# Performance work log

Hardware: AMD Instinct MI355X
Metric: run time of the kernel (lower is better)

Reference implementation:

```python
import jax, jax.numpy as jnp
import numpy as np

D_MODEL = 1024
N_HEADS = 16
D_K = D_MODEL // N_HEADS
CAUSAL = True


def setup_inputs() -> dict:
    key = jax.random.key(0)
    ks = jax.random.split(key, 11)
    B, S, D = 2, 2048, D_MODEL
    scale = 1.0 / np.sqrt(D)
    inp = {
        "in_Q": jax.random.normal(ks[0], (B, S, D), jnp.float32),
        "in_K": jax.random.normal(ks[1], (B, S, D), jnp.float32),
        "in_V": jax.random.normal(ks[2], (B, S, D), jnp.float32),
        # torch Linear params: weight [out, in], bias [out]
        "Wq": jax.random.normal(ks[3], (D, D), jnp.float32) * scale,
        "bq": jax.random.normal(ks[4], (D,), jnp.float32) * scale,
        "Wk": jax.random.normal(ks[5], (D, D), jnp.float32) * scale,
        "bk": jax.random.normal(ks[6], (D,), jnp.float32) * scale,
        "Wv": jax.random.normal(ks[7], (D, D), jnp.float32) * scale,
        "bv": jax.random.normal(ks[8], (D,), jnp.float32) * scale,
        "Wo": jax.random.normal(ks[9], (D, D), jnp.float32) * scale,
        "bo": jax.random.normal(ks[10], (D,), jnp.float32) * scale,
    }
    return inp


def reference(in_Q, in_K, in_V, Wq, bq, Wk, bk, Wv, bv, Wo, bo):
    B, S, D = in_Q.shape
    H, dk = N_HEADS, D_K
    # Linear projections (torch: x @ W.T + b)
    Q = in_Q @ Wq.T + bq
    K = in_K @ Wk.T + bk
    V = in_V @ Wv.T + bv
    # split heads: [B, S, D] -> [B, H, S, dk]
    Qh = Q.reshape(B, S, H, dk).transpose(0, 2, 1, 3)
    Kh = K.reshape(B, S, H, dk).transpose(0, 2, 1, 3)
    Vh = V.reshape(B, S, H, dk).transpose(0, 2, 1, 3)
    # scores [B, H, S, S]
    scores = jnp.einsum("bhqd,bhkd->bhqk", Qh, Kh) / jnp.sqrt(jnp.float32(dk))
    if CAUSAL:
        mask = jnp.tril(jnp.ones((S, S), dtype=bool))
        scores = jnp.where(mask, scores, -jnp.inf)
    attn = jax.nn.softmax(scores, axis=-1)
    out = jnp.einsum("bhqk,bhkd->bhqd", attn, Vh)
    Hcat = out.transpose(0, 2, 1, 3).reshape(B, S, D)
    return Hcat @ Wo.T + bo
```

## Files before the change

kernel.cpp:

```cpp
#include <hip/hip_runtime.h>
#include <hip/hip_bf16.h>
#include <math.h>

#define D_MODEL 1024
#define NHEADS  16
#define DK      64
#define SEQ     2048
#define BATCH   2
#define MROWS   4096
#define NQT     (SEQ/64)

typedef unsigned short ushort_t;
using short8 = __attribute__((ext_vector_type(8))) short;
using f32x4  = __attribute__((ext_vector_type(4))) float;

__device__ __forceinline__ ushort_t f2bf(float x) {
    unsigned u = __float_as_uint(x);
    u = (u + 0x7FFFu + ((u >> 16) & 1u)) >> 16;
    return (ushort_t)u;
}

__device__ __forceinline__ unsigned pk2(float a, float b) {
    __hip_bfloat162 h = __float22bfloat162_rn(float2{a, b});
    unsigned u;
    __builtin_memcpy(&u, &h, 4);
    return u;
}

__device__ __forceinline__ void gll16(const ushort_t* g, ushort_t* l) {
    __builtin_amdgcn_global_load_lds(
        (const __attribute__((address_space(1))) void*)(g),
        (__attribute__((address_space(3))) void*)(l), 16, 0, 0);
}

__global__ __launch_bounds__(256) void cvt_bf16(
    const float* s0, const float* s1, const float* s2, const float* s3,
    const float* s4, const float* s5, const float* s6,
    ushort_t* d0, ushort_t* d1, ushort_t* d2, ushort_t* d3,
    ushort_t* d4, ushort_t* d5, ushort_t* d6, int nIn, int nW)
{
    const float* s; ushort_t* d; int n;
    switch (blockIdx.y) {
        case 0: s = s0; d = d0; n = nIn; break;
        case 1: s = s1; d = d1; n = nIn; break;
        case 2: s = s2; d = d2; n = nIn; break;
        case 3: s = s3; d = d3; n = nW;  break;
        case 4: s = s4; d = d4; n = nW;  break;
        case 5: s = s5; d = d5; n = nW;  break;
        default: s = s6; d = d6; n = nW; break;
    }
    int i = (blockIdx.x * 256 + threadIdx.x) * 4;
    if (i < n) {
        float4 v = *(const float4*)&s[i];
        ushort4 o;
        o.x = f2bf(v.x); o.y = f2bf(v.y); o.z = f2bf(v.z); o.w = f2bf(v.w);
        *(ushort4*)&d[i] = o;
    }
}

struct GemmArgs { const ushort_t* A; const ushort_t* W; const float* bias;
                  void* C; int mode; float oscale; };

template<int MODE>
__device__ __forceinline__ void gemm_core(const GemmArgs& ga,
                                          ushort_t* As0, ushort_t* Bs0,
                                          ushort_t* As1, ushort_t* Bs1)
{
    constexpr bool SWP = (MODE != 1);
    const int tid  = threadIdx.x;
    const int w    = tid >> 6, lane = tid & 63;
    const int quad = lane >> 4, lx = lane & 15;
    const int mw = (w >> 1) * 64, nw = (w & 1) * 64;
    const int bm = blockIdx.x * 128, bn = blockIdx.y * 128;
    const int K = D_MODEL;

    auto stage = [&](int k0, ushort_t* As, ushort_t* Bs) {
#pragma unroll
        for (int i = 0; i < 4; ++i) {
            int r0 = (w * 4 + i) * 8;
            int rl = r0 + (lane >> 3);
            int g  = (lane & 7) ^ (rl & 7);
            gll16(&ga.A[(size_t)(bm + rl) * K + k0 + g * 8], &As[r0 * 64]);
            gll16(&ga.W[(size_t)(bn + rl) * K + k0 + g * 8], &Bs[r0 * 64]);
        }
    };

    f32x4 acc[4][4];
#pragma unroll
    for (int mt = 0; mt < 4; ++mt)
#pragma unroll
        for (int nt = 0; nt < 4; ++nt)
            acc[mt][nt] = (f32x4){0.f, 0.f, 0.f, 0.f};

    float4 b4[4];
    float  bfr[4];
#pragma unroll
    for (int nt = 0; nt < 4; ++nt) {
        if (SWP) b4[nt] = *(const float4*)&ga.bias[bn + nw + nt * 16 + quad * 4];
        else     bfr[nt] = ga.bias[bn + nw + nt * 16 + lx];
    }

    stage(0, As0, Bs0);

    for (int it = 0; it < K / 64; ++it) {
        ushort_t* As = (it & 1) ? As1 : As0;
        ushort_t* Bs = (it & 1) ? Bs1 : Bs0;

        asm volatile("s_waitcnt vmcnt(0)" ::: "memory");
        asm volatile("s_barrier" ::: "memory");

        if (it + 1 < K / 64)
            stage((it + 1) * 64, (it & 1) ? As0 : As1, (it & 1) ? Bs0 : Bs1);

#pragma unroll
        for (int ks = 0; ks < 2; ++ks) {
            short8 af[4], bf[4];
#pragma unroll
            for (int mt = 0; mt < 4; ++mt) {
                int r = mw + mt * 16 + lx;
                af[mt] = *(const short8*)&As[r * 64 + (((ks * 4 + quad) ^ (r & 7)) << 3)];
            }
#pragma unroll
            for (int nt = 0; nt < 4; ++nt) {
                int r = nw + nt * 16 + lx;
                bf[nt] = *(const short8*)&Bs[r * 64 + (((ks * 4 + quad) ^ (r & 7)) << 3)];
            }
#pragma unroll
            for (int mt = 0; mt < 4; ++mt)
#pragma unroll
                for (int nt = 0; nt < 4; ++nt)
                    acc[mt][nt] = SWP
                        ? __builtin_amdgcn_mfma_f32_16x16x32_bf16(bf[nt], af[mt], acc[mt][nt], 0, 0, 0)
                        : __builtin_amdgcn_mfma_f32_16x16x32_bf16(af[mt], bf[nt], acc[mt][nt], 0, 0, 0);
        }
    }

    if (MODE == 0) {
        ushort_t* C = (ushort_t*)ga.C;
        const float os = ga.oscale;
#pragma unroll
        for (int mt = 0; mt < 4; ++mt) {
            int m = bm + mw + mt * 16 + lx;
#pragma unroll
            for (int nt = 0; nt < 4; ++nt) {
                int n0 = bn + nw + nt * 16 + quad * 4;
                uint2 u;
                u.x = pk2((acc[mt][nt][0] + b4[nt].x) * os, (acc[mt][nt][1] + b4[nt].y) * os);
                u.y = pk2((acc[mt][nt][2] + b4[nt].z) * os, (acc[mt][nt][3] + b4[nt].w) * os);
                *(uint2*)&C[(size_t)m * D_MODEL + n0] = u;
            }
        }
    } else if (MODE == 2) {
        float* C = (float*)ga.C;
#pragma unroll
        for (int mt = 0; mt < 4; ++mt) {
            int m = bm + mw + mt * 16 + lx;
#pragma unroll
            for (int nt = 0; nt < 4; ++nt) {
                int n0 = bn + nw + nt * 16 + quad * 4;
                float4 v;
                v.x = acc[mt][nt][0] + b4[nt].x;
                v.y = acc[mt][nt][1] + b4[nt].y;
                v.z = acc[mt][nt][2] + b4[nt].z;
                v.w = acc[mt][nt][3] + b4[nt].w;
                *(float4*)&C[(size_t)m * D_MODEL + n0] = v;
            }
        }
    } else {
        ushort_t* C = (ushort_t*)ga.C;
#pragma unroll
        for (int mt = 0; mt < 4; ++mt)
#pragma unroll
            for (int nt = 0; nt < 4; ++nt) {
                int n = bn + nw + nt * 16 + lx;
                int d = n & 63, h = n >> 6;
                int m0 = bm + mw + mt * 16 + quad * 4;
                int b = m0 >> 11, s0 = m0 & 2047;
                uint2 u;
                u.x = pk2(acc[mt][nt][0] + bfr[nt], acc[mt][nt][1] + bfr[nt]);
                u.y = pk2(acc[mt][nt][2] + bfr[nt], acc[mt][nt][3] + bfr[nt]);
                *(uint2*)&C[((size_t)(b * NHEADS + h) * DK + d) * SEQ + s0] = u;
            }
    }
}

__global__ __launch_bounds__(256) void gemm_mfma(GemmArgs g0, GemmArgs g1, GemmArgs g2)
{
    __shared__ ushort_t As0[128 * 64], Bs0[128 * 64];
    __shared__ ushort_t As1[128 * 64], Bs1[128 * 64];
    GemmArgs ga = (blockIdx.z == 0) ? g0 : ((blockIdx.z == 1) ? g1 : g2);
    if (ga.mode == 0)      gemm_core<0>(ga, As0, Bs0, As1, Bs1);
    else if (ga.mode == 1) gemm_core<1>(ga, As0, Bs0, As1, Bs1);
    else                   gemm_core<2>(ga, As0, Bs0, As1, Bs1);
}

__device__ __forceinline__ void flash_tile(
    int qt, const size_t qbase, const size_t vbase,
    const ushort_t* __restrict__ Qp, const ushort_t* __restrict__ Kp,
    const ushort_t* __restrict__ Vt, ushort_t* __restrict__ Hc,
    ushort_t* Ks0, ushort_t* Ks1, ushort_t* Vs0, ushort_t* Vs1,
    ushort_t (*Ps)[16 * 72])
{
    const int tid  = threadIdx.x;
    const int w    = tid >> 6, lane = tid & 63;
    const int quad = lane >> 4, lx = lane & 15;

    asm volatile("s_barrier" ::: "memory");

    {
#pragma unroll
        for (int i = 0; i < 2; ++i) {
            int r0 = (w + i * 4) * 8;
            int rl = r0 + (lane >> 3);
            int g  = (lane & 7) ^ (rl & 7);
            gll16(&Kp[qbase + (size_t)rl * D_MODEL + g * 8], &Ks0[r0 * 64]);
            gll16(&Vt[vbase + (size_t)rl * SEQ + g * 8], &Vs0[r0 * 64]);
        }
    }

    short8 qf[2];
    {
        size_t ro = qbase + (size_t)(qt * 64 + w * 16 + lx) * D_MODEL + quad * 8;
        qf[0] = *(const short8*)&Qp[ro];
        qf[1] = *(const short8*)&Qp[ro + 32];
    }

    f32x4 O[4];
#pragma unroll
    for (int nt = 0; nt < 4; ++nt) O[nt] = (f32x4){0.f, 0.f, 0.f, 0.f};
    float mrow = -INFINITY, lrow = 0.f;
    const int qin = w * 16 + lx;

    for (int kt = 0; kt <= qt; ++kt) {
        ushort_t* Ks = (kt & 1) ? Ks1 : Ks0;
        ushort_t* Vs = (kt & 1) ? Vs1 : Vs0;

        asm volatile("s_waitcnt vmcnt(0)" ::: "memory");
        asm volatile("s_barrier" ::: "memory");

        if (kt < qt) {
            ushort_t* Kn = (kt & 1) ? Ks0 : Ks1;
            ushort_t* Vn = (kt & 1) ? Vs0 : Vs1;
#pragma unroll
            for (int i = 0; i < 2; ++i) {
                int r0 = (w + i * 4) * 8;
                int rl = r0 + (lane >> 3);
                int g  = (lane & 7) ^ (rl & 7);
                gll16(&Kp[qbase + (size_t)((kt + 1) * 64 + rl) * D_MODEL + g * 8], &Kn[r0 * 64]);
                gll16(&Vt[vbase + (size_t)rl * SEQ + (kt + 1) * 64 + g * 8], &Vn[r0 * 64]);
            }
        }

        f32x4 s[4];
#pragma unroll
        for (int nt = 0; nt < 4; ++nt) {
            int r = nt * 16 + lx;
            short8 kf0 = *(const short8*)&Ks[r * 64 + ((quad ^ (r & 7)) << 3)];
            short8 kf1 = *(const short8*)&Ks[r * 64 + (((4 + quad) ^ (r & 7)) << 3)];
            f32x4 z = (f32x4){0.f, 0.f, 0.f, 0.f};
            z = __builtin_amdgcn_mfma_f32_16x16x32_bf16(kf0, qf[0], z, 0, 0, 0);
            z = __builtin_amdgcn_mfma_f32_16x16x32_bf16(kf1, qf[1], z, 0, 0, 0);
            s[nt] = z;
        }

        if (kt == qt) {
#pragma unroll
            for (int nt = 0; nt < 4; ++nt)
#pragma unroll
                for (int r = 0; r < 4; ++r)
                    if ((nt * 16 + quad * 4 + r) > qin) s[nt][r] = -INFINITY;
        }

        float tm = -INFINITY;
#pragma unroll
        for (int nt = 0; nt < 4; ++nt)
#pragma unroll
            for (int r = 0; r < 4; ++r) tm = fmaxf(tm, s[nt][r]);
        tm = fmaxf(tm, __shfl_xor(tm, 16, 64));
        tm = fmaxf(tm, __shfl_xor(tm, 32, 64));
        float mnew = fmaxf(mrow, tm);
        float alpha = __builtin_amdgcn_exp2f(mrow - mnew);
        mrow = mnew;
        float rs = 0.f;
#pragma unroll
        for (int nt = 0; nt < 4; ++nt)
#pragma unroll
            for (int r = 0; r < 4; ++r) {
                float p = __builtin_amdgcn_exp2f(s[nt][r] - mnew);
                s[nt][r] = p;
                rs += p;
            }
        rs += __shfl_xor(rs, 16, 64);
        rs += __shfl_xor(rs, 32, 64);
        lrow = lrow * alpha + rs;
#pragma unroll
        for (int nt = 0; nt < 4; ++nt)
#pragma unroll
            for (int r = 0; r < 4; ++r) O[nt][r] *= alpha;

#pragma unroll
        for (int nt = 0; nt < 4; ++nt) {
            uint2 u;
            u.x = pk2(s[nt][0], s[nt][1]);
            u.y = pk2(s[nt][2], s[nt][3]);
            *(uint2*)&Ps[w][lx * 72 + nt * 16 + quad * 4] = u;
        }

        short8 pf0 = *(const short8*)&Ps[w][lx * 72 + quad * 8];
        short8 pf1 = *(const short8*)&Ps[w][lx * 72 + 32 + quad * 8];

#pragma unroll
        for (int nt = 0; nt < 4; ++nt) {
            int r = nt * 16 + lx;
            short8 vf0 = *(const short8*)&Vs[r * 64 + ((quad ^ (r & 7)) << 3)];
            short8 vf1 = *(const short8*)&Vs[r * 64 + (((4 + quad) ^ (r & 7)) << 3)];
            O[nt] = __builtin_amdgcn_mfma_f32_16x16x32_bf16(vf0, pf0, O[nt], 0, 0, 0);
            O[nt] = __builtin_amdgcn_mfma_f32_16x16x32_bf16(vf1, pf1, O[nt], 0, 0, 0);
        }
    }

    {
        float invl = 1.f / lrow;
        size_t ro = qbase + (size_t)(qt * 64 + w * 16 + lx) * D_MODEL;
#pragma unroll
        for (int nt = 0; nt < 4; ++nt) {
            uint2 u;
            u.x = pk2(O[nt][0] * invl, O[nt][1] * invl);
            u.y = pk2(O[nt][2] * invl, O[nt][3] * invl);
            *(uint2*)&Hc[ro + nt * 16 + quad * 4] = u;
        }
    }
}

__global__ __launch_bounds__(256) void flash_mfma(
    const ushort_t* __restrict__ Qp, const ushort_t* __restrict__ Kp,
    const ushort_t* __restrict__ Vt, ushort_t* __restrict__ Hc)
{
    const int id  = blockIdx.x;
    const int xcd = id & 7;
    const int k   = id >> 3;
    const int bh  = (xcd << 2) | (k & 3);
    const int p   = k >> 2;
    const int b = bh >> 4, h = bh & 15;

    __shared__ ushort_t Ks0[64 * 64], Ks1[64 * 64];
    __shared__ ushort_t Vs0[64 * 64], Vs1[64 * 64];
    __shared__ ushort_t Ps[4][16 * 72];

    const size_t qbase = (size_t)(b * SEQ) * D_MODEL + h * DK;
    const size_t vbase = (size_t)bh * DK * SEQ;

    flash_tile(NQT - 1 - p, qbase, vbase, Qp, Kp, Vt, Hc, Ks0, Ks1, Vs0, Vs1, Ps);
    flash_tile(p,           qbase, vbase, Qp, Kp, Vt, Hc, Ks0, Ks1, Vs0, Vs1, Ps);
}

extern "C" void kernel_launch(void* const* d_in, const int* in_sizes, int n_in,
                              void* d_out, int out_size, void* d_ws, size_t ws_size,
                              hipStream_t stream) {
    const float* inQ = (const float*)d_in[0];
    const float* inK = (const float*)d_in[1];
    const float* inV = (const float*)d_in[2];
    const float* Wq  = (const float*)d_in[3];
    const float* bq  = (const float*)d_in[4];
    const float* Wk  = (const float*)d_in[5];
    const float* bk  = (const float*)d_in[6];
    const float* Wv  = (const float*)d_in[7];
    const float* bv  = (const float*)d_in[8];
    const float* Wo  = (const float*)d_in[9];
    const float* bo  = (const float*)d_in[10];
    float* out = (float*)d_out;

    const size_t NI = (size_t)MROWS * D_MODEL;
    const size_t NW = (size_t)D_MODEL * D_MODEL;
    ushort_t* ws  = (ushort_t*)d_ws;
    ushort_t* Qb  = ws;
    ushort_t* Kb  = Qb  + NI;
    ushort_t* Vb  = Kb  + NI;
    ushort_t* Wqb = Vb  + NI;
    ushort_t* Wkb = Wqb + NW;
    ushort_t* Wvb = Wkb + NW;
    ushort_t* Wob = Wvb + NW;
    ushort_t* Qp  = Wob + NW;
    ushort_t* Kp  = Qp  + NI;
    ushort_t* Vtg = Kp  + NI;
    ushort_t* Hc  = Vtg + NI;

    cvt_bf16<<<dim3(NI / 1024, 7), 256, 0, stream>>>(
        inQ, inK, inV, Wq, Wk, Wv, Wo,
        Qb, Kb, Vb, Wqb, Wkb, Wvb, Wob, (int)NI, (int)NW);

    const float qsc = 0.125f * 1.44269504088896340736f;
    GemmArgs aq{Qb, Wqb, bq, (void*)Qp, 0, qsc};
    GemmArgs ak{Kb, Wkb, bk, (void*)Kp, 0, 1.0f};
    GemmArgs av{Vb, Wvb, bv, (void*)Vtg, 1, 1.0f};
    gemm_mfma<<<dim3(MROWS / 128, D_MODEL / 128, 3), 256, 0, stream>>>(aq, ak, av);

    flash_mfma<<<dim3(NQT / 2 * BATCH * NHEADS), 256, 0, stream>>>(Qp, Kp, Vtg, Hc);

    GemmArgs ao{Hc, Wob, bo, (void*)out, 2, 1.0f};
    gemm_mfma<<<dim3(MROWS / 128, D_MODEL / 128, 1), 256, 0, stream>>>(ao, ao, ao);
}
```

Baseline: 228.5 us.

## Add dedicated 64x128 output-projection GEMM and simplify flash grid mapping

Replaces the generic 128x128 mode-2 GEMM used for the output projection with a dedicated 64x128-tile kernel. This doubles the block count (512 instead of 256) so the MI355X CUs are better filled. The flash attention launch also changes from an XCD-aware swizzled 1D grid to a plain 2D grid (query-tile pair, batch-head). That gives up the explicit L2 locality of grouping heads per XCD. Smaller tiles lower data reuse per block in the output GEMM.

New measurement: 226.8 us. Within noise of the previous version (-0.7%).

```diff
diff --git a/kernel.cpp b/kernel.cpp
--- a/kernel.cpp
+++ b/kernel.cpp
@@ -150,22 +150,6 @@
                 *(uint2*)&C[(size_t)m * D_MODEL + n0] = u;
             }
         }
-    } else if (MODE == 2) {
-        float* C = (float*)ga.C;
-#pragma unroll
-        for (int mt = 0; mt < 4; ++mt) {
-            int m = bm + mw + mt * 16 + lx;
-#pragma unroll
-            for (int nt = 0; nt < 4; ++nt) {
-                int n0 = bn + nw + nt * 16 + quad * 4;
-                float4 v;
-                v.x = acc[mt][nt][0] + b4[nt].x;
-                v.y = acc[mt][nt][1] + b4[nt].y;
-                v.z = acc[mt][nt][2] + b4[nt].z;
-                v.w = acc[mt][nt][3] + b4[nt].w;
-                *(float4*)&C[(size_t)m * D_MODEL + n0] = v;
-            }
-        }
     } else {
         ushort_t* C = (ushort_t*)ga.C;
 #pragma unroll
@@ -189,9 +173,101 @@
     __shared__ ushort_t As0[128 * 64], Bs0[128 * 64];
     __shared__ ushort_t As1[128 * 64], Bs1[128 * 64];
     GemmArgs ga = (blockIdx.z == 0) ? g0 : ((blockIdx.z == 1) ? g1 : g2);
-    if (ga.mode == 0)      gemm_core<0>(ga, As0, Bs0, As1, Bs1);
-    else if (ga.mode == 1) gemm_core<1>(ga, As0, Bs0, As1, Bs1);
-    else                   gemm_core<2>(ga, As0, Bs0, As1, Bs1);
+    if (ga.mode == 0) gemm_core<0>(ga, As0, Bs0, As1, Bs1);
+    else              gemm_core<1>(ga, As0, Bs0, As1, Bs1);
+}
+
+__global__ __launch_bounds__(256) void gemm_o(
+    const ushort_t* __restrict__ A, const ushort_t* __restrict__ W,
+    const float* __restrict__ bias, float* __restrict__ C)
+{
+    __shared__ ushort_t As0[64 * 64],  As1[64 * 64];
+    __shared__ ushort_t Bs0[128 * 64], Bs1[128 * 64];
+
+    const int tid  = threadIdx.x;
+    const int w    = tid >> 6, lane = tid & 63;
+    const int quad = lane >> 4, lx = lane & 15;
+    const int mw = (w >> 1) * 32, nw = (w & 1) * 64;
+    const int bm = blockIdx.x * 64, bn = blockIdx.y * 128;
+    const int K = D_MODEL;
+
+    auto stage = [&](int k0, ushort_t* As, ushort_t* Bs) {
+#pragma unroll
+        for (int i = 0; i < 2; ++i) {
+            int r0 = (i * 4 + w) * 8;
+            int rl = r0 + (lane >> 3);
+            int g  = (lane & 7) ^ (rl & 7);
+            gll16(&A[(size_t)(bm + rl) * K + k0 + g * 8], &As[r0 * 64]);
+        }
+#pragma unroll
+        for (int i = 0; i < 4; ++i) {
+            int r0 = (i * 4 + w) * 8;
+            int rl = r0 + (lane >> 3);
+            int g  = (lane & 7) ^ (rl & 7);
+            gll16(&W[(size_t)(bn + rl) * K + k0 + g * 8], &Bs[r0 * 64]);
+        }
+    };
+
+    f32x4 acc[2][4];
+#pragma unroll
+    for (int mt = 0; mt < 2; ++mt)
+#pragma unroll
+        for (int nt = 0; nt < 4; ++nt)
+            acc[mt][nt] = (f32x4){0.f, 0.f, 0.f, 0.f};
+
+    float4 b4[4];
+#pragma unroll
+    for (int nt = 0; nt < 4; ++nt)
+        b4[nt] = *(const float4*)&bias[bn + nw + nt * 16 + quad * 4];
+
+    stage(0, As0, Bs0);
+
+    for (int it = 0; it < K / 64; ++it) {
+        ushort_t* As = (it & 1) ? As1 : As0;
+        ushort_t* Bs = (it & 1) ? Bs1 : Bs0;
+
+        asm volatile("s_waitcnt vmcnt(0)" ::: "memory");
+        asm volatile("s_barrier" ::: "memory");
+
+        if (it + 1 < K / 64)
+            stage((it + 1) * 64, (it & 1) ? As0 : As1, (it & 1) ? Bs0 : Bs1);
+
+#pragma unroll
+        for (int ks = 0; ks < 2; ++ks) {
+            short8 af[2], bf[4];
+#pragma unroll
+            for (int mt = 0; mt < 2; ++mt) {
+                int r = mw + mt * 16 + lx;
+                af[mt] = *(const short8*)&As[r * 64 + (((ks * 4 + quad) ^ (r & 7)) << 3)];
+            }
+#pragma unroll
+            for (int nt = 0; nt < 4; ++nt) {
+                int r = nw + nt * 16 + lx;
+                bf[nt] = *(const short8*)&Bs[r * 64 + (((ks * 4 + quad) ^ (r & 7)) << 3)];
+            }
+#pragma unroll
+            for (int mt = 0; mt < 2; ++mt)
+#pragma unroll
+                for (int nt = 0; nt < 4; ++nt)
+                    acc[mt][nt] = __builtin_amdgcn_mfma_f32_16x16x32_bf16(
+                        bf[nt], af[mt], acc[mt][nt], 0, 0, 0);
+        }
+    }
+
+#pragma unroll
+    for (int mt = 0; mt < 2; ++mt) {
+        int m = bm + mw + mt * 16 + lx;
+#pragma unroll
+        for (int nt = 0; nt < 4; ++nt) {
+            int n0 = bn + nw + nt * 16 + quad * 4;
+            float4 v;
+            v.x = acc[mt][nt][0] + b4[nt].x;
+            v.y = acc[mt][nt][1] + b4[nt].y;
+            v.z = acc[mt][nt][2] + b4[nt].z;
+            v.w = acc[mt][nt][3] + b4[nt].w;
+            *(float4*)&C[(size_t)m * D_MODEL + n0] = v;
+        }
+    }
 }
 
 __device__ __forceinline__ void flash_tile(
@@ -336,11 +412,8 @@
     const ushort_t* __restrict__ Qp, const ushort_t* __restrict__ Kp,
     const ushort_t* __restrict__ Vt, ushort_t* __restrict__ Hc)
 {
-    const int id  = blockIdx.x;
-    const int xcd = id & 7;
-    const int k   = id >> 3;
-    const int bh  = (xcd << 2) | (k & 3);
-    const int p   = k >> 2;
+    const int p  = blockIdx.x;
+    const int bh = blockIdx.y;
     const int b = bh >> 4, h = bh & 15;
 
     __shared__ ushort_t Ks0[64 * 64], Ks1[64 * 64];
@@ -395,8 +468,7 @@
     GemmArgs av{Vb, Wvb, bv, (void*)Vtg, 1, 1.0f};
     gemm_mfma<<<dim3(MROWS / 128, D_MODEL / 128, 3), 256, 0, stream>>>(aq, ak, av);
 
-    flash_mfma<<<dim3(NQT / 2 * BATCH * NHEADS), 256, 0, stream>>>(Qp, Kp, Vtg, Hc);
-
-    GemmArgs ao{Hc, Wob, bo, (void*)out, 2, 1.0f};
-    gemm_mfma<<<dim3(MROWS / 128, D_MODEL / 128, 1), 256, 0, stream>>>(ao, ao, ao);
-}
+    flash_mfma<<<dim3(NQT / 2, BATCH * NHEADS), 256, 0, stream>>>(Qp, Kp, Vtg, Hc);
+
+    gemm_o<<<dim3(MROWS / 64, D_MODEL / 128), 256, 0, stream>>>(Hc, Wob, bo, out);
+}
```
